# Performance work log

Measured on AMD Instinct MI355X. Metric: run time of the kernel, lower is better.

The kernel has to match this reference:

```python
import jax, jax.numpy as jnp
from jax import lax
import numpy as np

CHANNEL_N = 16
HIDDEN = 128
INPUT_CH = 1
KSIZE = 7
STEPS = 10
EPS = 1e-5


def setup_inputs() -> dict:
    key = jax.random.key(0)
    ks = jax.random.split(key, 8)
    B, H, W = 8, 256, 256
    x = jax.random.normal(ks[0], (B, H, W, CHANNEL_N), dtype=jnp.float32)
    # stochastic fire masks, one per step (torch: bernoulli_(p=fire_rate) under no_grad)
    masks = jax.random.bernoulli(ks[1], 0.5, (STEPS, B, 1, H, W))
    # depthwise conv: groups=channel_n -> weight [C,1,K,K]
    conv_w = jax.random.normal(ks[2], (CHANNEL_N, 1, KSIZE, KSIZE), dtype=jnp.float32) * 0.05
    conv_b = jax.random.normal(ks[3], (CHANNEL_N,), dtype=jnp.float32) * 0.05
    # fc0: 1x1 conv [hidden, 2*C]
    fc0_w = jax.random.normal(ks[4], (HIDDEN, 2 * CHANNEL_N), dtype=jnp.float32) * 0.1
    fc0_b = jax.random.normal(ks[5], (HIDDEN,), dtype=jnp.float32) * 0.05
    # fc1: 1x1 conv [C - input_channels, hidden], no bias (zero-init in torch; random here)
    fc1_w = jax.random.normal(ks[6], (CHANNEL_N - INPUT_CH, HIDDEN), dtype=jnp.float32) * 0.02
    bn_gamma = jnp.ones((HIDDEN,), dtype=jnp.float32)
    bn_beta = jnp.zeros((HIDDEN,), dtype=jnp.float32)
    return {"x": x, "masks": masks, "conv_w": conv_w, "conv_b": conv_b,
            "fc0_w": fc0_w, "fc0_b": fc0_b, "fc1_w": fc1_w,
            "bn_gamma": bn_gamma, "bn_beta": bn_beta}


def _nca_forward(x, masks, conv_w, conv_b, fc0_w, fc0_b, fc1_w, bn_gamma, bn_beta):
    state = jnp.transpose(x, (0, 3, 1, 2))  # b h w c -> b c h w
    const_in = state[:, :INPUT_CH]
    pad = (KSIZE - 1) // 2

    def step(state, mask):
        # depthwise 7x7 conv, reflect padding
        sp = jnp.pad(state, ((0, 0), (0, 0), (pad, pad), (pad, pad)), mode='reflect')
        d = lax.conv_general_dilated(
            sp, conv_w, window_strides=(1, 1), padding='VALID',
            dimension_numbers=('NCHW', 'OIHW', 'NCHW'),
            feature_group_count=CHANNEL_N)
        d = d + conv_b[None, :, None, None]
        cat = jnp.concatenate([state, d], axis=1)  # [B, 2C, H, W]
        # fc0 (1x1 conv)
        h = jnp.einsum('bchw,oc->bohw', cat, fc0_w) + fc0_b[None, :, None, None]
        # BatchNorm2d with batch statistics (track_running_stats=False)
        mean = jnp.mean(h, axis=(0, 2, 3), keepdims=True)
        var = jnp.var(h, axis=(0, 2, 3), keepdims=True)
        h = (h - mean) * lax.rsqrt(var + EPS)
        h = h * bn_gamma[None, :, None, None] + bn_beta[None, :, None, None]
        h = jax.nn.relu(h)
        # fc1 (1x1 conv, no bias)
        delta = jnp.einsum('bohw,ko->bkhw', h, fc1_w)  # [B, C-1, H, W]
        delta = delta * mask  # stochastic fire (broadcast over channels)
        new = state[:, INPUT_CH:] + delta
        return jnp.concatenate([const_in, new], axis=1), None

    state, _ = lax.scan(step, state, masks.astype(state.dtype))
    return jnp.transpose(state, (0, 2, 3, 1))  # b c h w -> b h w c


def reference(x, masks, conv_w, conv_b, fc0_w, fc0_b, fc1_w, bn_gamma, bn_beta):
    return _nca_forward(x, masks, conv_w, conv_b, fc0_w, fc0_b, fc1_w, bn_gamma, bn_beta)
```

## Files before the change

### kernel.cpp

```cpp
#include <hip/hip_runtime.h>

#define CH 16
#define HID 128
#define NB 8
#define NH 256
#define NW 256
#define NPX (NB*NH*NW)
#define NSTEP 10
#define GPW 8
#define KPW 2
#define SLAB 1280
#define NPART 64
#define PSTR 1088
#define POFF (NPART*PSTR)
#define STEPSTATS (POFF + 640)

typedef __attribute__((ext_vector_type(8))) short short8v;
typedef __attribute__((ext_vector_type(4))) float f32x4;

__device__ __forceinline__ int refl(int i, int n){
    if (i < 0) i = -i;
    if (i >= n) i = 2*n - 2 - i;
    return i;
}

__device__ __forceinline__ unsigned short f2bf(float x){
    unsigned int u = __float_as_uint(x);
    u += 0x7FFFu + ((u >> 16) & 1u);
    return (unsigned short)(u >> 16);
}
__device__ __forceinline__ float bf2f(unsigned short h){
    return __uint_as_float(((unsigned int)h) << 16);
}
__device__ __forceinline__ unsigned int cvtpk(float lo, float hi){
    unsigned int r;
    asm("v_cvt_pk_bf16_f32 %0, %1, %2" : "=v"(r) : "v"(lo), "v"(hi));
    return r;
}

__global__ void k_repack(const float* __restrict__ cw, const float* __restrict__ w0,
                         float* __restrict__ wp,
                         unsigned short* __restrict__ b0h, unsigned short* __restrict__ b0l){
    int t = blockIdx.x*256 + threadIdx.x;
    if (t < 49*16){ int tap = t >> 4, c = t & 15; wp[tap*16 + c] = cw[c*49 + tap]; }
    if (t < 4096){
        int n = t >> 9, l = (t >> 3) & 63, i = t & 7;
        int o = 16*n + (l & 15), k = ((l >> 4) << 3) + i;
        float v = w0[o*32 + k];
        unsigned short hi = f2bf(v);
        b0h[t] = hi;
        b0l[t] = f2bf(v - bf2f(hi));
    }
}

__global__ void k_zero(float* __restrict__ p, int n){
    int t = blockIdx.x*256 + threadIdx.x;
    if (t < n) p[t] = 0.f;
}

struct Row { float4 e[4]; float4 o[4]; };

__device__ __forceinline__ void fma4(float4& a, float4 w, float4 v){
    a.x += w.x*v.x; a.y += w.y*v.y; a.z += w.z*v.z; a.w += w.w*v.w;
}
__device__ __forceinline__ void ldrow(Row& r, const float4* L, int row, int tx){
    #pragma unroll
    for (int k=0;k<4;++k){
        r.e[k] = L[(row*2+0)*20 + tx + k];
        r.o[k] = L[(row*2+1)*20 + tx + k];
    }
}

__global__ __launch_bounds__(256,3)
void k_conv(const float* __restrict__ st, const float* __restrict__ wp,
            const float* __restrict__ cb, float* __restrict__ dout){
    __shared__ float4 tile4[38*2*20];
    __shared__ float4 cw4s[49];
    const int b = blockIdx.z >> 2, cg = blockIdx.z & 3;
    const int y0 = blockIdx.y*32, x0 = blockIdx.x*32;
    const int t = threadIdx.x;
    const int tx = t & 15, ty = t >> 4;

    if (t < 49) cw4s[t] = *(const float4*)&wp[t*16 + cg*4];
    for (int i = t; i < 38*38; i += 256){
        int py = i / 38, px = i - py*38;
        int gy = refl(y0 + py - 3, NH);
        int gx = refl(x0 + px - 3, NW);
        float4 v = *(const float4*)&st[(((size_t)b*NH + gy)*NW + gx)*CH + cg*4];
        tile4[(py*2 + (px&1))*20 + (px>>1)] = v;
    }
    __syncthreads();

    const float4* L = tile4;
    float4 bias = *(const float4*)&cb[cg*4];
    float4 a00 = bias, a01 = bias, a10 = bias, a11 = bias;
    Row A, B;
    ldrow(A, L, 2*ty,   tx);
    ldrow(B, L, 2*ty+1, tx);

#define CSTEP(dy, RA, RB, LOADNEXT, NR) \
    { \
        _Pragma("unroll") \
        for (int dx = 0; dx < 7; ++dx){ \
            float4 w4 = cw4s[(dy)*7 + dx]; \
            float4 v00 = ((dx)&1)   ? RA.o[(dx)>>1]   : RA.e[(dx)>>1]; \
            float4 v01 = ((dx+1)&1) ? RA.o[(dx+1)>>1] : RA.e[(dx+1)>>1]; \
            float4 v10 = ((dx)&1)   ? RB.o[(dx)>>1]   : RB.e[(dx)>>1]; \
            float4 v11 = ((dx+1)&1) ? RB.o[(dx+1)>>1] : RB.e[(dx+1)>>1]; \
            fma4(a00,w4,v00); fma4(a01,w4,v01); fma4(a10,w4,v10); fma4(a11,w4,v11); \
        } \
        if (LOADNEXT) ldrow(RA, L, NR, tx); \
    }

    CSTEP(0, A, B, 1, 2*ty+2)
    CSTEP(1, B, A, 1, 2*ty+3)
    CSTEP(2, A, B, 1, 2*ty+4)
    CSTEP(3, B, A, 1, 2*ty+5)
    CSTEP(4, A, B, 1, 2*ty+6)
    CSTEP(5, B, A, 1, 2*ty+7)
    CSTEP(6, A, B, 0, 0)
#undef CSTEP

    const size_t pr = ((size_t)b*NH + (size_t)(y0 + 2*ty))*NW + (x0 + 2*tx);
    *(float4*)&dout[(pr)*CH + cg*4]        = a00;
    *(float4*)&dout[(pr+1)*CH + cg*4]      = a01;
    *(float4*)&dout[(pr+NW)*CH + cg*4]     = a10;
    *(float4*)&dout[(pr+NW+1)*CH + cg*4]   = a11;
}

__global__ __launch_bounds__(512)
void k_stats(const float* __restrict__ st, const float* __restrict__ dv,
             float* __restrict__ S){
    __shared__ float lds[8*SLAB];
    const int t = threadIdx.x, lane = t & 63, w = t >> 6;
    const int lo = lane & 15, hi = lane >> 4;
    float* slab = &lds[w*SLAB];
    const int gw = blockIdx.x*8 + w;

    short8v ones;
    {
        short ov = (lo == 0) ? (short)0x3F80 : (short)0;
        #pragma unroll
        for (int i=0;i<8;++i) ones[i] = ov;
    }
    f32x4 a00 = (f32x4){0.f,0.f,0.f,0.f};
    f32x4 a01 = a00, a11 = a00, s0 = a00, s1 = a00;

    const int lp = lane >> 3, lq = lane & 7;
    const float* lbase = (lq < 4) ? st : dv;
    const int lch = (lq & 3) * 4;
    const size_t p0 = (size_t)gw * (KPW*32);

    float4 v[KPW][4];
    #pragma unroll
    for (int j=0;j<KPW;++j)
        #pragma unroll
        for (int j2=0;j2<4;++j2)
            v[j][j2] = *(const float4*)&lbase[(p0 + j*32 + lp + 8*j2)*CH + lch];

    #pragma unroll
    for (int j=0;j<KPW;++j){
        #pragma unroll
        for (int j2=0;j2<4;++j2){
            int p = lp + 8*j2;
            *(float2*)&slab[p*34 + lq*4]     = make_float2(v[j][j2].x, v[j][j2].y);
            *(float2*)&slab[p*34 + lq*4 + 2] = make_float2(v[j][j2].z, v[j][j2].w);
        }
        short8v r0h, r0l, r1h, r1l;
        #pragma unroll
        for (int ct=0;ct<2;++ct){
            #pragma unroll
            for (int i=0;i<8;++i){
                float f = slab[(hi*8+i)*34 + ct*16 + lo];
                unsigned int u = __float_as_uint(f);
                unsigned short ah = (unsigned short)(u >> 16);
                float r = f - __uint_as_float(u & 0xFFFF0000u);
                unsigned short al = (unsigned short)(__float_as_uint(r) >> 16);
                if (ct==0){ r0h[i]=(short)ah; r0l[i]=(short)al; }
                else      { r1h[i]=(short)ah; r1l[i]=(short)al; }
            }
        }
        s0 = __builtin_amdgcn_mfma_f32_16x16x32_bf16(ones, r0h, s0, 0,0,0);
        s0 = __builtin_amdgcn_mfma_f32_16x16x32_bf16(ones, r0l, s0, 0,0,0);
        s1 = __builtin_amdgcn_mfma_f32_16x16x32_bf16(ones, r1h, s1, 0,0,0);
        s1 = __builtin_amdgcn_mfma_f32_16x16x32_bf16(ones, r1l, s1, 0,0,0);
        a00 = __builtin_amdgcn_mfma_f32_16x16x32_bf16(r0h, r0h, a00, 0,0,0);
        a00 = __builtin_amdgcn_mfma_f32_16x16x32_bf16(r0l, r0h, a00, 0,0,0);
        a00 = __builtin_amdgcn_mfma_f32_16x16x32_bf16(r0h, r0l, a00, 0,0,0);
        a11 = __builtin_amdgcn_mfma_f32_16x16x32_bf16(r1h, r1h, a11, 0,0,0);
        a11 = __builtin_amdgcn_mfma_f32_16x16x32_bf16(r1l, r1h, a11, 0,0,0);
        a11 = __builtin_amdgcn_mfma_f32_16x16x32_bf16(r1h, r1l, a11, 0,0,0);
        a01 = __builtin_amdgcn_mfma_f32_16x16x32_bf16(r0h, r1h, a01, 0,0,0);
        a01 = __builtin_amdgcn_mfma_f32_16x16x32_bf16(r0l, r1h, a01, 0,0,0);
        a01 = __builtin_amdgcn_mfma_f32_16x16x32_bf16(r0h, r1l, a01, 0,0,0);
    }

    float* red = lds;
    #pragma unroll
    for (int k=0;k<4;++k){
        red[t*20 + k]      = a00[k];
        red[t*20 + 4 + k]  = a01[k];
        red[t*20 + 8 + k]  = a11[k];
        red[t*20 + 12 + k] = s0[k];
        red[t*20 + 16 + k] = s1[k];
    }
    __syncthreads();
    if (w == 0){
        float tmp[20];
        #pragma unroll
        for (int k=0;k<20;++k){
            float s = 0.f;
            #pragma unroll
            for (int ww=0;ww<8;++ww) s += red[(lane + 64*ww)*20 + k];
            tmp[k] = s;
        }
        float* part = S + (size_t)(blockIdx.x & (NPART-1))*PSTR;
        #pragma unroll
        for (int r=0;r<4;++r){
            atomicAdd(&part[(hi*4+r)*32 + lo],        tmp[r]);
            atomicAdd(&part[(hi*4+r)*32 + 16 + lo],   tmp[4+r]);
            atomicAdd(&part[(16+hi*4+r)*32 + 16+lo],  tmp[8+r]);
        }
        if (hi == 0){
            atomicAdd(&part[1024 + lo],      tmp[12]);
            atomicAdd(&part[1024 + 16 + lo], tmp[16]);
        }
    }
}

__global__ void k_finalize(const float* __restrict__ Sin,
                           const float* __restrict__ w0, const float* __restrict__ b0,
                           const float* __restrict__ gam, const float* __restrict__ bet,
                           const float* __restrict__ f1, float* __restrict__ Sout){
    __shared__ float Ssm[1056];
    const int t = threadIdx.x;
    for (int e = t; e < 1056; e += 512){
        float s = 0.f;
        #pragma unroll 4
        for (int p = 0; p < NPART; ++p) s += Sin[(size_t)p*PSTR + e];
        Ssm[e] = s;
    }
    __syncthreads();
    if (t < 128){
        const int o = t;
        const float inv = 1.f / (float)NPX;
        float w[32];
        #pragma unroll
        for (int c=0;c<32;++c) w[c] = w0[o*32+c];
        float m1 = 0.f;
        #pragma unroll
        for (int c=0;c<32;++c) m1 += w[c]*Ssm[1024+c];
        m1 *= inv;
        float q = 0.f;
        #pragma unroll
        for (int i=0;i<32;++i){
            float ti = 0.f;
            #pragma unroll
            for (int j=0;j<32;++j){
                float sv = (i >= 16 && j < 16) ? Ssm[j*32+i] : Ssm[i*32+j];
                ti += sv*w[j];
            }
            q += w[i]*ti;
        }
        q *= inv;
        float var = q - m1*m1;
        float rstd = rsqrtf(var + 1e-5f);
        float mean = m1 + b0[o];
        float scale = rstd * gam[o];
        Sout[POFF + o] = bet[o]/scale + b0[o] - mean;
        unsigned short* f1sh = (unsigned short*)(Sout + POFF + 128);
        const int base = (o>>5)*512 + ((o>>3)&3)*128 + (o&7);
        f1sh[base] = 0;
        #pragma unroll
        for (int c=1;c<16;++c)
            f1sh[base + c*8] = f2bf(f1[(c-1)*HID + o] * scale);
    }
}

__global__ __launch_bounds__(256)
void k_update(const float* __restrict__ st, const float* __restrict__ dv,
              const int* __restrict__ msk,
              const unsigned short* __restrict__ gb0h, const unsigned short* __restrict__ gb0l,
              const float* __restrict__ Sstep, float* __restrict__ out){
    __shared__ __align__(16) unsigned int hls[4*16*68];
    const int lane = threadIdx.x & 63, w = threadIdx.x >> 6;
    const int lo16 = lane & 15, qw = lane >> 4;
    unsigned int* hb = &hls[w*16*68];

    const short8v* p0h = (const short8v*)gb0h;
    const short8v* p0l = (const short8v*)gb0l;
    const short8v* p1h = (const short8v*)(Sstep + POFF + 128);
    short8v B0h[8], B0l[8], B1h[4];
    #pragma unroll
    for (int n=0;n<8;++n){ B0h[n] = p0h[n*64 + lane]; B0l[n] = p0l[n*64 + lane]; }
    #pragma unroll
    for (int tt=0;tt<4;++tt) B1h[tt] = p1h[tt*64 + lane];
    const float* shb = Sstep + POFF;
    float4 shbv[8];
    #pragma unroll
    for (int n=0;n<8;++n) shbv[n] = *(const float4*)&shb[16*n + 4*qw];

    const int gw = blockIdx.x*4 + w;
    const float* abase = (qw < 2) ? st : dv;
    const int choff = (qw & 1)*8;

    for (int gi = 0; gi < GPW; ++gi){
        const size_t pg0 = ((size_t)gw*GPW + gi)*16;
        const float* ap = abase + (pg0 + lo16)*CH + choff;
        float4 v0 = *(const float4*)ap;
        float4 v1 = *(const float4*)(ap + 4);
        float av[8] = {v0.x,v0.y,v0.z,v0.w,v1.x,v1.y,v1.z,v1.w};
        short8v ah, al;
        #pragma unroll
        for (int i=0;i<8;++i){
            unsigned int u = __float_as_uint(av[i]);
            ah[i] = (short)(unsigned short)(u >> 16);
            float r = av[i] - __uint_as_float(u & 0xFFFF0000u);
            al[i] = (short)(unsigned short)(__float_as_uint(r) >> 16);
        }
        f32x4 acc[8];
        #pragma unroll
        for (int n=0;n<8;++n)
            acc[n] = (f32x4){shbv[n].x, shbv[n].y, shbv[n].z, shbv[n].w};
        #pragma unroll
        for (int n=0;n<8;++n){
            acc[n] = __builtin_amdgcn_mfma_f32_16x16x32_bf16(B0h[n], ah, acc[n], 0,0,0);
            acc[n] = __builtin_amdgcn_mfma_f32_16x16x32_bf16(B0h[n], al, acc[n], 0,0,0);
            acc[n] = __builtin_amdgcn_mfma_f32_16x16x32_bf16(B0l[n], ah, acc[n], 0,0,0);
        }
        #pragma unroll
        for (int n=0;n<8;++n){
            float h0 = fmaxf(acc[n][0], 0.f), h1 = fmaxf(acc[n][1], 0.f);
            float h2 = fmaxf(acc[n][2], 0.f), h3 = fmaxf(acc[n][3], 0.f);
            unsigned int wa = cvtpk(h0, h1), wb = cvtpk(h2, h3);
            *(uint2*)&hb[lo16*68 + 8*n + 2*qw] = make_uint2(wa, wb);
        }
        f32x4 dacc = (f32x4){0.f,0.f,0.f,0.f};
        #pragma unroll
        for (int tt=0;tt<4;++tt){
            short8v ah2 = *(const short8v*)&hb[lo16*68 + 16*tt + 4*qw];
            dacc = __builtin_amdgcn_mfma_f32_16x16x32_bf16(B1h[tt], ah2, dacc, 0,0,0);
        }
        const size_t p = pg0 + lo16;
        float4 stv = *(const float4*)&st[p*CH + 4*qw];
        const float m = (float)msk[p];
        float4 ov;
        ov.x = stv.x + dacc[0]*m;
        ov.y = stv.y + dacc[1]*m;
        ov.z = stv.z + dacc[2]*m;
        ov.w = stv.w + dacc[3]*m;
        *(float4*)&out[p*CH + 4*qw] = ov;
    }
}

extern "C" void kernel_launch(void* const* d_in, const int* in_sizes, int n_in,
                              void* d_out, int out_size, void* d_ws, size_t ws_size,
                              hipStream_t stream){
    const float* x   = (const float*)d_in[0];
    const int*   mk  = (const int*)d_in[1];
    const float* cw  = (const float*)d_in[2];
    const float* cb  = (const float*)d_in[3];
    const float* w0  = (const float*)d_in[4];
    const float* b0  = (const float*)d_in[5];
    const float* f1  = (const float*)d_in[6];
    const float* gam = (const float*)d_in[7];
    const float* bet = (const float*)d_in[8];

    float* ws    = (float*)d_ws;
    float* dbuf  = ws;
    float* sbuf  = ws + (size_t)NPX*CH;
    float* stats = ws + (size_t)2*NPX*CH;
    float* wp    = stats + (size_t)NSTEP*STEPSTATS;
    unsigned short* b0h = (unsigned short*)(wp + 800);
    unsigned short* b0l = b0h + 4096;

    k_repack<<<16,256,0,stream>>>(cw, w0, wp, b0h, b0l);
    k_zero<<<(NSTEP*STEPSTATS+255)/256,256,0,stream>>>(stats, NSTEP*STEPSTATS);

    const float* cur = x;
    float* outp = (float*)d_out;
    for (int s=0;s<NSTEP;++s){
        float* S = stats + (size_t)s*STEPSTATS;
        float* nxt = (s & 1) ? outp : sbuf;
        k_conv<<<dim3(NW/32,NH/32,NB*4),256,0,stream>>>(cur, wp, cb, dbuf);
        k_stats<<<1024,512,0,stream>>>(cur, dbuf, S);
        k_finalize<<<1,512,0,stream>>>(S, w0, b0, gam, bet, f1, S);
        k_update<<<NPX/16/4/GPW,256,0,stream>>>(cur, dbuf, mk + (size_t)s*NPX,
                                                b0h, b0l, S, nxt);
        cur = nxt;
    }
}
```

Measured before the change: 1.095 ms.

## Fuse BN finalize into update kernel and halve stats partial buckets

Removes the single-block finalize kernel. Each update block now reduces the per-step stat partials into shared memory, computes the BN shift and scaled fc1 weights itself, and stores them in LDS. The number of atomic partial buckets is halved so each block has less to sum. This saves a launch and a serial single-block stage per step. In exchange, every update block repeats the reduction and the quadratic-form work, and the atomics in the stats kernel see more contention.

```diff
diff --git a/kernel.cpp b/kernel.cpp
--- a/kernel.cpp
+++ b/kernel.cpp
@@ -10,10 +10,10 @@
 #define GPW 8
 #define KPW 2
 #define SLAB 1280
-#define NPART 64
+#define NPART 32
 #define PSTR 1088
-#define POFF (NPART*PSTR)
-#define STEPSTATS (POFF + 640)
+#define STEPSTATS (NPART*PSTR)
+#define SBLK 1024
 
 typedef __attribute__((ext_vector_type(8))) short short8v;
 typedef __attribute__((ext_vector_type(4))) float f32x4;
@@ -228,77 +228,73 @@
     }
 }
 
-__global__ void k_finalize(const float* __restrict__ Sin,
-                           const float* __restrict__ w0, const float* __restrict__ b0,
-                           const float* __restrict__ gam, const float* __restrict__ bet,
-                           const float* __restrict__ f1, float* __restrict__ Sout){
-    __shared__ float Ssm[1056];
-    const int t = threadIdx.x;
-    for (int e = t; e < 1056; e += 512){
-        float s = 0.f;
-        #pragma unroll 4
-        for (int p = 0; p < NPART; ++p) s += Sin[(size_t)p*PSTR + e];
-        Ssm[e] = s;
-    }
-    __syncthreads();
-    if (t < 128){
-        const int o = t;
-        const float inv = 1.f / (float)NPX;
-        float w[32];
-        #pragma unroll
-        for (int c=0;c<32;++c) w[c] = w0[o*32+c];
-        float m1 = 0.f;
-        #pragma unroll
-        for (int c=0;c<32;++c) m1 += w[c]*Ssm[1024+c];
-        m1 *= inv;
-        float q = 0.f;
-        #pragma unroll
-        for (int i=0;i<32;++i){
-            float ti = 0.f;
-            #pragma unroll
-            for (int j=0;j<32;++j){
-                float sv = (i >= 16 && j < 16) ? Ssm[j*32+i] : Ssm[i*32+j];
-                ti += sv*w[j];
-            }
-            q += w[i]*ti;
-        }
-        q *= inv;
-        float var = q - m1*m1;
-        float rstd = rsqrtf(var + 1e-5f);
-        float mean = m1 + b0[o];
-        float scale = rstd * gam[o];
-        Sout[POFF + o] = bet[o]/scale + b0[o] - mean;
-        unsigned short* f1sh = (unsigned short*)(Sout + POFF + 128);
-        const int base = (o>>5)*512 + ((o>>3)&3)*128 + (o&7);
-        f1sh[base] = 0;
-        #pragma unroll
-        for (int c=1;c<16;++c)
-            f1sh[base + c*8] = f2bf(f1[(c-1)*HID + o] * scale);
-    }
-}
-
 __global__ __launch_bounds__(256)
 void k_update(const float* __restrict__ st, const float* __restrict__ dv,
               const int* __restrict__ msk,
               const unsigned short* __restrict__ gb0h, const unsigned short* __restrict__ gb0l,
-              const float* __restrict__ Sstep, float* __restrict__ out){
-    __shared__ __align__(16) unsigned int hls[4*16*68];
+              const float* __restrict__ Sp,
+              const float* __restrict__ w0g, const float* __restrict__ b0,
+              const float* __restrict__ gam, const float* __restrict__ bet,
+              const float* __restrict__ f1, float* __restrict__ out){
+    __shared__ __align__(16) unsigned int scratch[4*16*68];
+    __shared__ float fin[128];
+    __shared__ __align__(16) unsigned short f1s_l[2048];
+
+    {
+        float* Ssm = (float*)scratch;
+        for (int e = threadIdx.x; e < 1056; e += 256){
+            float s = 0.f;
+            #pragma unroll 8
+            for (int p = 0; p < NPART; ++p) s += Sp[(size_t)p*PSTR + e];
+            Ssm[e] = s;
+        }
+        __syncthreads();
+        if (threadIdx.x < 128){
+            const int o = threadIdx.x;
+            const float inv = 1.f / (float)NPX;
+            float m1 = 0.f, q = 0.f;
+            #pragma unroll 1
+            for (int i=0;i<32;++i){
+                float wi = w0g[o*32+i];
+                m1 += wi*Ssm[1024+i];
+                float ti = 0.f;
+                #pragma unroll 8
+                for (int j=0;j<32;++j){
+                    float sv = (i >= 16 && j < 16) ? Ssm[j*32+i] : Ssm[i*32+j];
+                    ti += sv * w0g[o*32+j];
+                }
+                q += wi*ti;
+            }
+            m1 *= inv; q *= inv;
+            float var = q - m1*m1;
+            float rstd = rsqrtf(var + 1e-5f);
+            float mean = m1 + b0[o];
+            float scale = rstd * gam[o];
+            fin[o] = bet[o]/scale + b0[o] - mean;
+            const int base = (o>>5)*512 + ((o>>3)&3)*128 + (o&7);
+            f1s_l[base] = 0;
+            #pragma unroll
+            for (int c=1;c<16;++c)
+                f1s_l[base + c*8] = f2bf(f1[(c-1)*HID + o] * scale);
+        }
+        __syncthreads();
+    }
+
     const int lane = threadIdx.x & 63, w = threadIdx.x >> 6;
     const int lo16 = lane & 15, qw = lane >> 4;
-    unsigned int* hb = &hls[w*16*68];
+    unsigned int* hb = &scratch[w*16*68];
 
     const short8v* p0h = (const short8v*)gb0h;
     const short8v* p0l = (const short8v*)gb0l;
-    const short8v* p1h = (const short8v*)(Sstep + POFF + 128);
+    const short8v* p1h = (const short8v*)f1s_l;
     short8v B0h[8], B0l[8], B1h[4];
     #pragma unroll
     for (int n=0;n<8;++n){ B0h[n] = p0h[n*64 + lane]; B0l[n] = p0l[n*64 + lane]; }
     #pragma unroll
     for (int tt=0;tt<4;++tt) B1h[tt] = p1h[tt*64 + lane];
-    const float* shb = Sstep + POFF;
     float4 shbv[8];
     #pragma unroll
-    for (int n=0;n<8;++n) shbv[n] = *(const float4*)&shb[16*n + 4*qw];
+    for (int n=0;n<8;++n) shbv[n] = *(const float4*)&fin[16*n + 4*qw];
 
     const int gw = blockIdx.x*4 + w;
     const float* abase = (qw < 2) ? st : dv;
@@ -383,10 +379,9 @@
         float* S = stats + (size_t)s*STEPSTATS;
         float* nxt = (s & 1) ? outp : sbuf;
         k_conv<<<dim3(NW/32,NH/32,NB*4),256,0,stream>>>(cur, wp, cb, dbuf);
-        k_stats<<<1024,512,0,stream>>>(cur, dbuf, S);
-        k_finalize<<<1,512,0,stream>>>(S, w0, b0, gam, bet, f1, S);
+        k_stats<<<SBLK,512,0,stream>>>(cur, dbuf, S);
         k_update<<<NPX/16/4/GPW,256,0,stream>>>(cur, dbuf, mk + (size_t)s*NPX,
-                                                b0h, b0l, S, nxt);
+                                                b0h, b0l, S, w0, b0, gam, bet, f1, nxt);
         cur = nxt;
     }
 }
```

Result: slower. 1.601 ms (+46.3%).
